# Performance work log

Hardware: AMD Instinct MI355X
Metric: run time of the kernel (lower is better)

## Reference

```python
import jax, jax.numpy as jnp
import numpy as np

N = 50000
E = 800000
IN_C = 16
H = 64
EA = 3
L = 3
EPS = 1e-5

def layer_norm(h, g, b):
    mu = jnp.mean(h, axis=-1, keepdims=True)
    var = jnp.var(h, axis=-1, keepdims=True)
    return (h - mu) * jax.lax.rsqrt(var + EPS) * g + b

def setup_inputs() -> dict:
    key = jax.random.key(0)
    ks = jax.random.split(key, 24)
    s = lambda *sh: 0.05
    d = {}
    d["x"] = jax.random.normal(ks[0], (N, IN_C), jnp.float32)
    d["edge_index"] = jax.random.randint(ks[1], (2, E), 0, N, jnp.int32)
    d["edge_attr"] = jax.random.normal(ks[2], (E, EA), jnp.float32)
    # encoder
    d["enc_w"] = jax.random.normal(ks[3], (IN_C, H), jnp.float32) * 0.1
    d["enc_b"] = jnp.zeros((H,), jnp.float32)
    d["enc_ln_g"] = jnp.ones((H,), jnp.float32)
    d["enc_ln_b"] = jnp.zeros((H,), jnp.float32)
    # message-passing MLPs (stacked over layers)
    d["mlp_w1"] = jax.random.normal(ks[4], (L, H + EA, H // 2), jnp.float32) * 0.1
    d["mlp_b1"] = jnp.zeros((L, H // 2), jnp.float32)
    d["mlp_w2"] = jax.random.normal(ks[5], (L, H // 2, H), jnp.float32) * 0.1
    d["mlp_b2"] = jnp.zeros((L, H), jnp.float32)
    d["ln_g"] = jnp.ones((L, H), jnp.float32)
    d["ln_b"] = jnp.zeros((L, H), jnp.float32)
    # heads
    d["depth_w1"] = jax.random.normal(ks[6], (H, H // 2), jnp.float32) * 0.1
    d["depth_b1"] = jnp.zeros((H // 2,), jnp.float32)
    d["depth_w2"] = jax.random.normal(ks[7], (H // 2, 1), jnp.float32) * 0.1
    d["depth_b2"] = jnp.zeros((1,), jnp.float32)
    d["vel_w1"] = jax.random.normal(ks[8], (H, H // 2), jnp.float32) * 0.1
    d["vel_b1"] = jnp.zeros((H // 2,), jnp.float32)
    d["vel_w2"] = jax.random.normal(ks[9], (H // 2, 2), jnp.float32) * 0.1
    d["vel_b2"] = jnp.zeros((2,), jnp.float32)
    return d

def reference(x, edge_index, edge_attr, enc_w, enc_b, enc_ln_g, enc_ln_b,
              mlp_w1, mlp_b1, mlp_w2, mlp_b2, ln_g, ln_b,
              depth_w1, depth_b1, depth_w2, depth_b2,
              vel_w1, vel_b1, vel_w2, vel_b2):
    src, dst = edge_index[0], edge_index[1]  # PyG: x_j = x[src], aggregate at dst
    # encoder (dropout inactive in eval mode)
    h = layer_norm(x @ enc_w + enc_b, enc_ln_g, enc_ln_b)
    h = jax.nn.relu(h)
    # in-degree counts for mean aggregation (isolated nodes -> 0, like PyG)
    cnt = jax.ops.segment_sum(jnp.ones((E,), jnp.float32), dst, num_segments=N)
    inv_cnt = jnp.where(cnt > 0, 1.0 / jnp.maximum(cnt, 1.0), 0.0)[:, None]
    for i in range(L):
        m_in = jnp.concatenate([h[src], edge_attr], axis=1)          # [E, H+EA]
        m = jax.nn.relu(m_in @ mlp_w1[i] + mlp_b1[i]) @ mlp_w2[i] + mlp_b2[i]  # [E, H]
        agg = jax.ops.segment_sum(m, dst, num_segments=N) * inv_cnt  # mean aggregate
        h = layer_norm(h + agg, ln_g[i], ln_b[i])
    depth = jax.nn.relu(h @ depth_w1 + depth_b1) @ depth_w2 + depth_b2    # [N,1]
    velocity = jax.nn.relu(h @ vel_w1 + vel_b1) @ vel_w2 + vel_b2         # [N,2]
    return (depth, velocity)
```

## Files before the change

kernel.cpp:

```cpp
#include <hip/hip_runtime.h>
#include <hip/hip_bf16.h>
#include <hip/hip_fp16.h>

typedef __hip_bfloat16 bf16;
typedef unsigned int u32;
typedef float f4v __attribute__((ext_vector_type(4)));

#define NN 50000
#define NE 800000
#define INC 16
#define HD 64
#define EPSV 1e-5f
#define NB1 196

__device__ __forceinline__ float b2f(bf16 v) { return __bfloat162float(v); }
__device__ __forceinline__ bool is_bf(const void* det) {
  return *(const u32*)det == 0x3F803F80u;
}

__device__ __forceinline__ float4 ldnt4(const float4* p) {
  f4v t = __builtin_nontemporal_load(reinterpret_cast<const f4v*>(p));
  float4 r; r.x = t[0]; r.y = t[1]; r.z = t[2]; r.w = t[3];
  return r;
}

template<typename T> __device__ __forceinline__ float ldv(const T* p, int i);
template<> __device__ __forceinline__ float ldv<float>(const float* p, int i) { return p[i]; }
template<> __device__ __forceinline__ float ldv<bf16>(const bf16* p, int i) { return b2f(p[i]); }

#define W1F   0
#define B1F   6432
#define W2F   6528
#define B2F   12672
#define DW1F  12864
#define DB1F  14912
#define DW2F  14944
#define DB2F  14976
#define VW1F  14977
#define VB1F  17025
#define VW2F  17057
#define VB2F  17121
#define WFTOT 17123

#define H_OFF    0
#define P0_OFF   3200000
#define CSR_OFF  4800000
#define WF_OFF   8000000
#define CNTI_OFF (WF_OFF + WFTOT)
#define RS_OFF   (CNTI_OFF + NN)
#define BSUM_OFF (RS_OFF + NN)
#define BOFF_OFF (BSUM_OFF + 256)
#define LPOS_OFF (BOFF_OFF + 256)
#define INV_OFF  (LPOS_OFF + NE)
#define P1_OFF   (INV_OFF + NE)
#define WS_NEED_ROOMY ((size_t)(P1_OFF + NN * 16) * 4)

template<typename T>
__device__ __forceinline__ void prep_body(
    const T* w1, const T* b1, const T* w2, const T* b2,
    const T* dw1, const T* db1, const T* dw2, const T* db2,
    const T* vw1, const T* vb1, const T* vw2, const T* vb2,
    float* wf, int i) {
  float v;
  if      (i < B1F)  v = ldv(w1,  i - W1F);
  else if (i < W2F)  v = ldv(b1,  i - B1F);
  else if (i < B2F)  v = ldv(w2,  i - W2F);
  else if (i < DW1F) v = ldv(b2,  i - B2F);
  else if (i < DB1F) v = ldv(dw1, i - DW1F);
  else if (i < DW2F) v = ldv(db1, i - DB1F);
  else if (i < DB2F) v = ldv(dw2, i - DW2F);
  else if (i < VW1F) v = ldv(db2, i - DB2F);
  else if (i < VB1F) v = ldv(vw1, i - VW1F);
  else if (i < VW2F) v = ldv(vb1, i - VB1F);
  else if (i < VB2F) v = ldv(vw2, i - VW2F);
  else               v = ldv(vb2, i - VB2F);
  wf[i] = v;
}

__global__ __launch_bounds__(256) void prep_kernel(
    const void* w1, const void* b1, const void* w2, const void* b2,
    const void* dw1, const void* db1, const void* dw2, const void* db2,
    const void* vw1, const void* vb1, const void* vw2, const void* vb2,
    float* __restrict__ wf, const void* __restrict__ det) {
  int i = blockIdx.x * blockDim.x + threadIdx.x;
  if (i >= WFTOT) return;
  if (is_bf(det))
    prep_body((const bf16*)w1, (const bf16*)b1, (const bf16*)w2, (const bf16*)b2,
              (const bf16*)dw1, (const bf16*)db1, (const bf16*)dw2, (const bf16*)db2,
              (const bf16*)vw1, (const bf16*)vb1, (const bf16*)vw2, (const bf16*)vb2, wf, i);
  else
    prep_body((const float*)w1, (const float*)b1, (const float*)w2, (const float*)b2,
              (const float*)dw1, (const float*)db1, (const float*)dw2, (const float*)db2,
              (const float*)vw1, (const float*)vb1, (const float*)vw2, (const float*)vb2, wf, i);
}

__global__ __launch_bounds__(256) void encoder_kernel(
    const void* __restrict__ x, const void* __restrict__ enc_w,
    const void* __restrict__ enc_b, const void* __restrict__ g,
    const void* __restrict__ b, float* __restrict__ h,
    __half* __restrict__ pout, const float* __restrict__ nw1,
    const float* __restrict__ nb1, const void* __restrict__ det) {
  __shared__ float shv[4][64];
  int node = (blockIdx.x * blockDim.x + threadIdx.x) >> 6;
  int lane = threadIdx.x & 63;
  int w = threadIdx.x >> 6;
  if (node >= NN) return;
  int jl = lane & 31, half = lane >> 5;
  float xv[INC], wv[INC], ebv, gv, bv;
  if (is_bf(det)) {
    const bf16* xp = (const bf16*)x + node * INC;
    const bf16* wp = (const bf16*)enc_w;
    #pragma unroll
    for (int k = 0; k < INC; k++) { xv[k] = b2f(xp[k]); wv[k] = b2f(wp[k * HD + lane]); }
    ebv = b2f(((const bf16*)enc_b)[lane]);
    gv  = b2f(((const bf16*)g)[lane]);
    bv  = b2f(((const bf16*)b)[lane]);
  } else {
    const float* xp = (const float*)x + node * INC;
    const float* wp = (const float*)enc_w;
    #pragma unroll
    for (int k = 0; k < INC; k++) { xv[k] = xp[k]; wv[k] = wp[k * HD + lane]; }
    ebv = ((const float*)enc_b)[lane];
    gv  = ((const float*)g)[lane];
    bv  = ((const float*)b)[lane];
  }
  float acc = ebv;
  #pragma unroll
  for (int k = 0; k < INC; k++) acc += xv[k] * wv[k];
  float s1 = acc, s2 = acc * acc;
  #pragma unroll
  for (int o = 32; o; o >>= 1) { s1 += __shfl_xor(s1, o); s2 += __shfl_xor(s2, o); }
  float mu = s1 * (1.0f / 64.0f);
  float var = fmaxf(s2 * (1.0f / 64.0f) - mu * mu, 0.0f);
  float d = acc - mu;
  float hv = fmaxf(d * rsqrtf(var + EPSV) * gv + bv, 0.0f);
  h[node * HD + lane] = hv;
  shv[w][lane] = hv;
  float pacc = 0.0f;
  int kb = half << 5;
  #pragma unroll
  for (int k4 = 0; k4 < 32; k4 += 4) {
    float4 h4 = *reinterpret_cast<const float4*>(&shv[w][kb + k4]);
    int kk = kb + k4;
    pacc += h4.x * nw1[kk * 32 + jl] + h4.y * nw1[(kk + 1) * 32 + jl]
          + h4.z * nw1[(kk + 2) * 32 + jl] + h4.w * nw1[(kk + 3) * 32 + jl];
  }
  pacc += __shfl_xor(pacc, 32);
  if (half == 0) pout[node * 32 + jl] = __float2half(pacc + nb1[jl]);
}

__global__ __launch_bounds__(256) void count_kernel(const int* __restrict__ ei,
                                                    int* __restrict__ cnt,
                                                    int* __restrict__ lpos) {
  int e = blockIdx.x * blockDim.x + threadIdx.x;
  if (e < NE) lpos[e] = atomicAdd(&cnt[ei[NE + e]], 1);
}

__global__ __launch_bounds__(256) void scan1_kernel(const int* __restrict__ cnt,
                                                    int* __restrict__ ex,
                                                    int* __restrict__ bsum) {
  __shared__ int s[256];
  int t = threadIdx.x, idx = blockIdx.x * 256 + t;
  int v = (idx < NN) ? cnt[idx] : 0;
  s[t] = v;
  __syncthreads();
  #pragma unroll
  for (int off = 1; off < 256; off <<= 1) {
    int u = (t >= off) ? s[t - off] : 0;
    __syncthreads();
    s[t] += u;
    __syncthreads();
  }
  if (idx < NN) ex[idx] = s[t] - v;
  if (t == 255) bsum[blockIdx.x] = s[255];
}

__global__ __launch_bounds__(256) void scan2_kernel(int* __restrict__ bsum,
                                                    int* __restrict__ boff) {
  __shared__ int s[256];
  int t = threadIdx.x;
  int v = (t < NB1) ? bsum[t] : 0;
  s[t] = v;
  __syncthreads();
  #pragma unroll
  for (int off = 1; off < 256; off <<= 1) {
    int u = (t >= off) ? s[t - off] : 0;
    __syncthreads();
    s[t] += u;
    __syncthreads();
  }
  boff[t] = s[t] - v;
}

__global__ __launch_bounds__(256) void scan3_kernel(int* __restrict__ rs,
                                                    const int* __restrict__ boff) {
  int idx = blockIdx.x * 256 + threadIdx.x;
  if (idx >= NN) return;
  rs[idx] += boff[blockIdx.x];
}

__global__ __launch_bounds__(256) void inv_kernel(const int* __restrict__ ei,
                                                  const int* __restrict__ rs,
                                                  const int* __restrict__ lpos,
                                                  int* __restrict__ inv) {
  int e = blockIdx.x * blockDim.x + threadIdx.x;
  if (e >= NE) return;
  int dst = ei[NE + e];
  inv[rs[dst] + lpos[e]] = e;
}

__global__ __launch_bounds__(256) void fill_kernel(const int* __restrict__ inv,
                                                   const int* __restrict__ ei,
                                                   const void* __restrict__ attr,
                                                   float4* __restrict__ csr,
                                                   const void* __restrict__ det) {
  int p = blockIdx.x * blockDim.x + threadIdx.x;
  if (p >= NE) return;
  int e = inv[p];
  int src = ei[e];
  float a0, a1, a2;
  if (is_bf(det)) {
    const bf16* ap = (const bf16*)attr + 3 * e;
    a0 = b2f(ap[0]); a1 = b2f(ap[1]); a2 = b2f(ap[2]);
  } else {
    const float* ap = (const float*)attr + 3 * e;
    a0 = ap[0]; a1 = ap[1]; a2 = ap[2];
  }
  float4 v; v.x = a0; v.y = a1; v.z = a2; v.w = __int_as_float(src);
  csr[p] = v;
}

__global__ __launch_bounds__(256) void node_pre_kernel(
    const float* __restrict__ h, const float* __restrict__ w1,
    const float* __restrict__ b1, __half* __restrict__ p) {
  int t = blockIdx.x * blockDim.x + threadIdx.x;
  int node = t >> 5;
  int j = t & 31;
  if (node >= NN) return;
  const float* hr = h + node * HD;
  float acc = b1[j];
  #pragma unroll
  for (int k = 0; k < HD; k++) acc += hr[k] * w1[k * 32 + j];
  p[node * 32 + j] = __float2half(acc);
}

__global__ __launch_bounds__(128) void gather_kernel(
    float* __restrict__ h, const __half2* __restrict__ pin,
    __half* __restrict__ pnext, const float4* __restrict__ csr,
    const int* __restrict__ rs, const int* __restrict__ cnt,
    const float* __restrict__ w1a, const float* __restrict__ w2,
    const float* __restrict__ b2v, const void* __restrict__ gbase,
    const void* __restrict__ bbase, int layer,
    const float* __restrict__ nw1, const float* __restrict__ nb1,
    int do_pnext, const float* __restrict__ wf, void* __restrict__ out,
    const void* __restrict__ det) {
  __shared__ float sacc[2][2][32];
  __shared__ float shv[2][2][64];
  int wid = (blockIdx.x * blockDim.x + threadIdx.x) >> 6;
  int lane = threadIdx.x & 63;
  int w = threadIdx.x >> 6;
  int n0 = 2 * wid, n1 = 2 * wid + 1;
  if (n0 >= NN) return;
  int jl = lane & 31, half = lane >> 5;
  int q4 = lane >> 4, pp = lane & 15;
  float2 wa0 = *reinterpret_cast<const float2*>(&w1a[2 * pp]);
  float2 wa1 = *reinterpret_cast<const float2*>(&w1a[32 + 2 * pp]);
  float2 wa2 = *reinterpret_cast<const float2*>(&w1a[64 + 2 * pp]);
  int s0 = rs[n0], c0 = cnt[n0];
  int s1 = rs[n1], c1 = cnt[n1];
  float hres0 = h[n0 * HD + lane];
  float hres1 = h[n1 * HD + lane];
  float b2l = b2v[lane];

  bool isbf = is_bf(det);
  int gidx = layer * HD + lane;
  float gv, bv;
  if (isbf) {
    gv = b2f(((const bf16*)gbase)[gidx]);
    bv = b2f(((const bf16*)bbase)[gidx]);
  } else {
    gv = ((const float*)gbase)[gidx];
    bv = ((const float*)bbase)[gidx];
  }

  int cm10 = (c0 > 0) ? c0 - 1 : 0;
  int cm11 = (c1 > 0) ? c1 - 1 : 0;
  int t0 = (c0 > 0) ? s0 : 0;
  int t1 = (c1 > 0) ? s1 : 0;

  float2 acc0 = make_float2(0.f, 0.f), acc1 = make_float2(0.f, 0.f);
  int cmax = max(c0, c1);
  if (cmax > 0) {
    float4 e0[4], e1[4];
    #pragma unroll
    for (int t = 0; t < 4; t++) {
      e0[t] = ldnt4(&csr[t0 + min(4 * t + q4, cm10)]);
      e1[t] = ldnt4(&csr[t1 + min(4 * t + q4, cm11)]);
    }
    for (int b0 = 0; b0 < cmax; b0 += 16) {
      float2 g0[4], g1[4];
      #pragma unroll
      for (int t = 0; t < 4; t++)
        g0[t] = __half22float2(pin[__float_as_int(e0[t].w) * 16 + pp]);
      #pragma unroll
      for (int t = 0; t < 4; t++)
        g1[t] = __half22float2(pin[__float_as_int(e1[t].w) * 16 + pp]);
      float2 pa0[4], pa1[4];
      #pragma unroll
      for (int t = 0; t < 4; t++) {
        pa0[t].x = e0[t].x * wa0.x + e0[t].y * wa1.x + e0[t].z * wa2.x;
        pa0[t].y = e0[t].x * wa0.y + e0[t].y * wa1.y + e0[t].z * wa2.y;
        pa1[t].x = e1[t].x * wa0.x + e1[t].y * wa1.x + e1[t].z * wa2.x;
        pa1[t].y = e1[t].x * wa0.y + e1[t].y * wa1.y + e1[t].z * wa2.y;
      }
      int nb = b0 + 16;
      if (nb < cmax) {
        #pragma unroll
        for (int t = 0; t < 4; t++) {
          e0[t] = ldnt4(&csr[t0 + min(nb + 4 * t + q4, cm10)]);
          e1[t] = ldnt4(&csr[t1 + min(nb + 4 * t + q4, cm11)]);
        }
      }
      #pragma unroll
      for (int t = 0; t < 4; t++) {
        int eo = b0 + 4 * t + q4;
        float rx0 = fmaxf(g0[t].x + pa0[t].x, 0.0f);
        float ry0 = fmaxf(g0[t].y + pa0[t].y, 0.0f);
        acc0.x += (eo < c0) ? rx0 : 0.0f;
        acc0.y += (eo < c0) ? ry0 : 0.0f;
        float rx1 = fmaxf(g1[t].x + pa1[t].x, 0.0f);
        float ry1 = fmaxf(g1[t].y + pa1[t].y, 0.0f);
        acc1.x += (eo < c1) ? rx1 : 0.0f;
        acc1.y += (eo < c1) ? ry1 : 0.0f;
      }
    }
  }
  acc0.x += __shfl_xor(acc0.x, 16); acc0.y += __shfl_xor(acc0.y, 16);
  acc1.x += __shfl_xor(acc1.x, 16); acc1.y += __shfl_xor(acc1.y, 16);
  acc0.x += __shfl_xor(acc0.x, 32); acc0.y += __shfl_xor(acc0.y, 32);
  acc1.x += __shfl_xor(acc1.x, 32); acc1.y += __shfl_xor(acc1.y, 32);
  if (lane < 16) {
    *reinterpret_cast<float2*>(&sacc[w][0][2 * pp]) = acc0;
    *reinterpret_cast<float2*>(&sacc[w][1][2 * pp]) = acc1;
  }

  float m0 = 0.0f, m1 = 0.0f;
  #pragma unroll
  for (int j4 = 0; j4 < 32; j4 += 4) {
    float4 a0 = *reinterpret_cast<const float4*>(&sacc[w][0][j4]);
    float4 a1 = *reinterpret_cast<const float4*>(&sacc[w][1][j4]);
    float w20 = w2[(j4 + 0) * HD + lane], w21 = w2[(j4 + 1) * HD + lane];
    float w22 = w2[(j4 + 2) * HD + lane], w23 = w2[(j4 + 3) * HD + lane];
    m0 += a0.x * w20 + a0.y * w21 + a0.z * w22 + a0.w * w23;
    m1 += a1.x * w20 + a1.y * w21 + a1.z * w22 + a1.w * w23;
  }
  float aggv0 = (c0 > 0) ? (m0 / (float)c0 + b2l) : 0.0f;
  float aggv1 = (c1 > 0) ? (m1 / (float)c1 + b2l) : 0.0f;

  float v0 = hres0 + aggv0, v1 = hres1 + aggv1;
  float s10 = v0, s20 = v0 * v0, s11 = v1, s21 = v1 * v1;
  #pragma unroll
  for (int o = 32; o; o >>= 1) {
    s10 += __shfl_xor(s10, o); s20 += __shfl_xor(s20, o);
    s11 += __shfl_xor(s11, o); s21 += __shfl_xor(s21, o);
  }
  float mu0 = s10 * (1.0f / 64.0f), mu1 = s11 * (1.0f / 64.0f);
  float var0 = fmaxf(s20 * (1.0f / 64.0f) - mu0 * mu0, 0.0f);
  float var1 = fmaxf(s21 * (1.0f / 64.0f) - mu1 * mu1, 0.0f);
  float hv0 = (v0 - mu0) * rsqrtf(var0 + EPSV) * gv + bv;
  float hv1 = (v1 - mu1) * rsqrtf(var1 + EPSV) * gv + bv;

  shv[w][0][lane] = hv0;
  shv[w][1][lane] = hv1;

  if (do_pnext) {
    float p0a = 0.0f, p1a = 0.0f;
    int kb = half << 5;
    #pragma unroll
    for (int k4 = 0; k4 < 32; k4 += 4) {
      float4 h0 = *reinterpret_cast<const float4*>(&shv[w][0][kb + k4]);
      float4 h1 = *reinterpret_cast<const float4*>(&shv[w][1][kb + k4]);
      int kk = kb + k4;
      float n0v = nw1[kk * 32 + jl], n1v = nw1[(kk + 1) * 32 + jl];
      float n2v = nw1[(kk + 2) * 32 + jl], n3v = nw1[(kk + 3) * 32 + jl];
      p0a += h0.x * n0v + h0.y * n1v + h0.z * n2v + h0.w * n3v;
      p1a += h1.x * n0v + h1.y * n1v + h1.z * n2v + h1.w * n3v;
    }
    p0a += __shfl_xor(p0a, 32);
    p1a += __shfl_xor(p1a, 32);
    if (half == 0) {
      pnext[n0 * 32 + jl] = __float2half(p0a + nb1[jl]);
      pnext[n1 * 32 + jl] = __float2half(p1a + nb1[jl]);
    }
  }

  if (layer == 2) {
    const float* w1h = wf + (half ? VW1F : DW1F);
    float a20 = half ? wf[VB1F + jl] : wf[DB1F + jl];
    float a21 = a20;
    #pragma unroll
    for (int k4 = 0; k4 < 64; k4 += 4) {
      float4 h0 = *reinterpret_cast<const float4*>(&shv[w][0][k4]);
      float4 h1 = *reinterpret_cast<const float4*>(&shv[w][1][k4]);
      float wv0 = w1h[(k4 + 0) * 32 + jl], wv1 = w1h[(k4 + 1) * 32 + jl];
      float wv2 = w1h[(k4 + 2) * 32 + jl], wv3 = w1h[(k4 + 3) * 32 + jl];
      a20 += h0.x * wv0 + h0.y * wv1 + h0.z * wv2 + h0.w * wv3;
      a21 += h1.x * wv0 + h1.y * wv1 + h1.z * wv2 + h1.w * wv3;
    }
    a20 = fmaxf(a20, 0.0f);
    a21 = fmaxf(a21, 0.0f);
    float r00, r10, r01, r11;
    if (half == 0) {
      r00 = a20 * wf[DW2F + jl]; r10 = 0.0f;
      r01 = a21 * wf[DW2F + jl]; r11 = 0.0f;
    } else {
      r00 = a20 * wf[VW2F + 2 * jl]; r10 = a20 * wf[VW2F + 2 * jl + 1];
      r01 = a21 * wf[VW2F + 2 * jl]; r11 = a21 * wf[VW2F + 2 * jl + 1];
    }
    #pragma unroll
    for (int o = 16; o; o >>= 1) {
      r00 += __shfl_xor(r00, o); r10 += __shfl_xor(r10, o);
      r01 += __shfl_xor(r01, o); r11 += __shfl_xor(r11, o);
    }
    if (lane == 0) {
      float d0 = r00 + wf[DB2F];
      float d1 = r01 + wf[DB2F];
      if (isbf) {
        ((bf16*)out)[n0] = __float2bfloat16(d0);
        ((bf16*)out)[n1] = __float2bfloat16(d1);
      } else {
        ((float*)out)[n0] = d0;
        ((float*)out)[n1] = d1;
      }
    }
    if (lane == 32) {
      float v00 = r00 + wf[VB2F], v01 = r10 + wf[VB2F + 1];
      float v10 = r01 + wf[VB2F], v11 = r11 + wf[VB2F + 1];
      if (isbf) {
        ((bf16*)out)[NN + 2 * n0]     = __float2bfloat16(v00);
        ((bf16*)out)[NN + 2 * n0 + 1] = __float2bfloat16(v01);
        ((bf16*)out)[NN + 2 * n1]     = __float2bfloat16(v10);
        ((bf16*)out)[NN + 2 * n1 + 1] = __float2bfloat16(v11);
      } else {
        ((float*)out)[NN + 2 * n0]     = v00;
        ((float*)out)[NN + 2 * n0 + 1] = v01;
        ((float*)out)[NN + 2 * n1]     = v10;
        ((float*)out)[NN + 2 * n1 + 1] = v11;
      }
    }
  } else {
    h[n0 * HD + lane] = hv0;
    h[n1 * HD + lane] = hv1;
  }
}

extern "C" void kernel_launch(void* const* d_in, const int* in_sizes, int n_in,
                              void* d_out, int out_size, void* d_ws, size_t ws_size,
                              hipStream_t stream) {
  const void* x     = d_in[0];
  const int*  ei    = (const int*)d_in[1];
  const void* attr  = d_in[2];
  const void* enc_w = d_in[3];
  const void* enc_b = d_in[4];
  const void* enc_g = d_in[5];
  const void* enc_bb= d_in[6];
  const void* mw1   = d_in[7];
  const void* mb1   = d_in[8];
  const void* mw2   = d_in[9];
  const void* mb2   = d_in[10];
  const void* lng   = d_in[11];
  const void* lnb   = d_in[12];
  const void* dw1   = d_in[13];
  const void* db1   = d_in[14];
  const void* dw2   = d_in[15];
  const void* db2   = d_in[16];
  const void* vw1   = d_in[17];
  const void* vb1   = d_in[18];
  const void* vw2   = d_in[19];
  const void* vb2   = d_in[20];

  float* ws    = (float*)d_ws;
  float* h     = ws + H_OFF;
  __half* p0   = (__half*)(ws + P0_OFF);
  float4* csr  = (float4*)(ws + CSR_OFF);
  float* wf    = ws + WF_OFF;
  int*   cnti  = (int*)(ws + CNTI_OFF);
  int*   rs    = (int*)(ws + RS_OFF);
  int*   bsum  = (int*)(ws + BSUM_OFF);
  int*   boff  = (int*)(ws + BOFF_OFF);
  int*   lpos  = (int*)(ws + LPOS_OFF);
  int*   inv   = (int*)(ws + INV_OFF);
  __half* p1   = (__half*)(ws + P1_OFF);
  bool roomy = ws_size >= WS_NEED_ROOMY;

  hipMemsetAsync(cnti, 0, (size_t)NN * sizeof(int), stream);
  prep_kernel<<<(WFTOT + 255) / 256, 256, 0, stream>>>(
      mw1, mb1, mw2, mb2, dw1, db1, dw2, db2, vw1, vb1, vw2, vb2, wf, enc_g);
  encoder_kernel<<<(NN + 3) / 4, 256, 0, stream>>>(
      x, enc_w, enc_b, enc_g, enc_bb, h, p0, wf + W1F, wf + B1F, enc_g);
  count_kernel<<<(NE + 255) / 256, 256, 0, stream>>>(ei, cnti, lpos);
  scan1_kernel<<<NB1, 256, 0, stream>>>(cnti, rs, bsum);
  scan2_kernel<<<1, 256, 0, stream>>>(bsum, boff);
  scan3_kernel<<<NB1, 256, 0, stream>>>(rs, boff);
  inv_kernel<<<(NE + 255) / 256, 256, 0, stream>>>(ei, rs, lpos, inv);
  fill_kernel<<<(NE + 255) / 256, 256, 0, stream>>>(inv, ei, attr, csr, enc_g);

  for (int l = 0; l < 3; l++) {
    __half* pin  = (roomy && (l & 1)) ? p1 : p0;
    __half* pnxt = (roomy && !(l & 1)) ? p1 : p0;
    if (!roomy && l > 0) {
      node_pre_kernel<<<(NN * 32 + 255) / 256, 256, 0, stream>>>(
          h, wf + W1F + l * 2144, wf + B1F + l * 32, p0);
      pin = p0; pnxt = p0;
    }
    int do_pnext = (roomy && l < 2) ? 1 : 0;
    int nl = (l < 2) ? l + 1 : l;
    gather_kernel<<<(NN + 3) / 4, 128, 0, stream>>>(
        h, (const __half2*)pin, pnxt, csr, rs, cnti,
        wf + W1F + l * 2144 + 64 * 32, wf + W2F + l * 2048, wf + B2F + l * 64,
        lng, lnb, l,
        wf + W1F + nl * 2144, wf + B1F + nl * 32, do_pnext,
        wf, d_out, enc_g);
  }
}
```

Before: 344.9 us.

## Process four nodes per wavefront in gather and fuse count into encoder

The gather kernel now handles four destination nodes per 64-lane wavefront instead of two, with 256-thread blocks, vectorized int4 loads of row starts and counts, and 16 outstanding CSR/gather loads per lane for more memory-level parallelism. The in-degree count kernel is merged into the encoder launch as extra blocks, removing one launch and letting the two independent jobs overlap. The trade-offs are higher register pressure (which may lower occupancy) and more divergence from unequal degrees, since each wave loops to the largest degree of its four nodes.

Result: slower. 478.3 us (+38.7%).

```diff
diff --git a/kernel.cpp b/kernel.cpp
--- a/kernel.cpp
+++ b/kernel.cpp
@@ -12,6 +12,8 @@
 #define HD 64
 #define EPSV 1e-5f
 #define NB1 196
+#define CNTB 3125
+#define ENCB 12500
 
 __device__ __forceinline__ float b2f(bf16 v) { return __bfloat162float(v); }
 __device__ __forceinline__ bool is_bf(const void* det) {
@@ -94,14 +96,21 @@
               (const float*)vw1, (const float*)vb1, (const float*)vw2, (const float*)vb2, wf, i);
 }
 
-__global__ __launch_bounds__(256) void encoder_kernel(
+__global__ __launch_bounds__(256) void enc_count_kernel(
     const void* __restrict__ x, const void* __restrict__ enc_w,
     const void* __restrict__ enc_b, const void* __restrict__ g,
     const void* __restrict__ b, float* __restrict__ h,
     __half* __restrict__ pout, const float* __restrict__ nw1,
-    const float* __restrict__ nb1, const void* __restrict__ det) {
+    const float* __restrict__ nb1, const int* __restrict__ ei,
+    int* __restrict__ cnt, int* __restrict__ lpos,
+    const void* __restrict__ det) {
+  if (blockIdx.x < CNTB) {
+    int e = blockIdx.x * 256 + threadIdx.x;
+    if (e < NE) lpos[e] = atomicAdd(&cnt[ei[NE + e]], 1);
+    return;
+  }
   __shared__ float shv[4][64];
-  int node = (blockIdx.x * blockDim.x + threadIdx.x) >> 6;
+  int node = ((blockIdx.x - CNTB) * blockDim.x + threadIdx.x) >> 6;
   int lane = threadIdx.x & 63;
   int w = threadIdx.x >> 6;
   if (node >= NN) return;
@@ -147,13 +156,6 @@
   }
   pacc += __shfl_xor(pacc, 32);
   if (half == 0) pout[node * 32 + jl] = __float2half(pacc + nb1[jl]);
-}
-
-__global__ __launch_bounds__(256) void count_kernel(const int* __restrict__ ei,
-                                                    int* __restrict__ cnt,
-                                                    int* __restrict__ lpos) {
-  int e = blockIdx.x * blockDim.x + threadIdx.x;
-  if (e < NE) lpos[e] = atomicAdd(&cnt[ei[NE + e]], 1);
 }
 
 __global__ __launch_bounds__(256) void scan1_kernel(const int* __restrict__ cnt,
@@ -244,7 +246,7 @@
   p[node * 32 + j] = __float2half(acc);
 }
 
-__global__ __launch_bounds__(128) void gather_kernel(
+__global__ __launch_bounds__(256) void gather_kernel(
     float* __restrict__ h, const __half2* __restrict__ pin,
     __half* __restrict__ pnext, const float4* __restrict__ csr,
     const int* __restrict__ rs, const int* __restrict__ cnt,
@@ -254,22 +256,25 @@
     const float* __restrict__ nw1, const float* __restrict__ nb1,
     int do_pnext, const float* __restrict__ wf, void* __restrict__ out,
     const void* __restrict__ det) {
-  __shared__ float sacc[2][2][32];
-  __shared__ float shv[2][2][64];
+  __shared__ float sacc[4][4][32];
+  __shared__ float shv[4][4][64];
   int wid = (blockIdx.x * blockDim.x + threadIdx.x) >> 6;
   int lane = threadIdx.x & 63;
   int w = threadIdx.x >> 6;
-  int n0 = 2 * wid, n1 = 2 * wid + 1;
+  int n0 = 4 * wid;
   if (n0 >= NN) return;
   int jl = lane & 31, half = lane >> 5;
   int q4 = lane >> 4, pp = lane & 15;
   float2 wa0 = *reinterpret_cast<const float2*>(&w1a[2 * pp]);
   float2 wa1 = *reinterpret_cast<const float2*>(&w1a[32 + 2 * pp]);
   float2 wa2 = *reinterpret_cast<const float2*>(&w1a[64 + 2 * pp]);
-  int s0 = rs[n0], c0 = cnt[n0];
-  int s1 = rs[n1], c1 = cnt[n1];
-  float hres0 = h[n0 * HD + lane];
-  float hres1 = h[n1 * HD + lane];
+  int4 s4 = *reinterpret_cast<const int4*>(&rs[n0]);
+  int4 c4 = *reinterpret_cast<const int4*>(&cnt[n0]);
+  int sA[4] = {s4.x, s4.y, s4.z, s4.w};
+  int cA[4] = {c4.x, c4.y, c4.z, c4.w};
+  float hres[4];
+  #pragma unroll
+  for (int n = 0; n < 4; n++) hres[n] = h[(n0 + n) * HD + lane];
   float b2l = b2v[lane];
 
   bool isbf = is_bf(det);
@@ -283,174 +288,192 @@
     bv = ((const float*)bbase)[gidx];
   }
 
-  int cm10 = (c0 > 0) ? c0 - 1 : 0;
-  int cm11 = (c1 > 0) ? c1 - 1 : 0;
-  int t0 = (c0 > 0) ? s0 : 0;
-  int t1 = (c1 > 0) ? s1 : 0;
-
-  float2 acc0 = make_float2(0.f, 0.f), acc1 = make_float2(0.f, 0.f);
-  int cmax = max(c0, c1);
+  int tA[4], cmA[4];
+  #pragma unroll
+  for (int n = 0; n < 4; n++) {
+    cmA[n] = (cA[n] > 0) ? cA[n] - 1 : 0;
+    tA[n]  = (cA[n] > 0) ? sA[n] : 0;
+  }
+
+  float2 acc[4];
+  #pragma unroll
+  for (int n = 0; n < 4; n++) acc[n] = make_float2(0.f, 0.f);
+  int cmax = max(max(cA[0], cA[1]), max(cA[2], cA[3]));
   if (cmax > 0) {
-    float4 e0[4], e1[4];
-    #pragma unroll
-    for (int t = 0; t < 4; t++) {
-      e0[t] = ldnt4(&csr[t0 + min(4 * t + q4, cm10)]);
-      e1[t] = ldnt4(&csr[t1 + min(4 * t + q4, cm11)]);
+    float4 e[4][4];
+    #pragma unroll
+    for (int n = 0; n < 4; n++) {
+      #pragma unroll
+      for (int t = 0; t < 4; t++)
+        e[n][t] = ldnt4(&csr[tA[n] + min(4 * t + q4, cmA[n])]);
     }
     for (int b0 = 0; b0 < cmax; b0 += 16) {
-      float2 g0[4], g1[4];
-      #pragma unroll
-      for (int t = 0; t < 4; t++)
-        g0[t] = __half22float2(pin[__float_as_int(e0[t].w) * 16 + pp]);
-      #pragma unroll
-      for (int t = 0; t < 4; t++)
-        g1[t] = __half22float2(pin[__float_as_int(e1[t].w) * 16 + pp]);
-      float2 pa0[4], pa1[4];
-      #pragma unroll
-      for (int t = 0; t < 4; t++) {
-        pa0[t].x = e0[t].x * wa0.x + e0[t].y * wa1.x + e0[t].z * wa2.x;
-        pa0[t].y = e0[t].x * wa0.y + e0[t].y * wa1.y + e0[t].z * wa2.y;
-        pa1[t].x = e1[t].x * wa0.x + e1[t].y * wa1.x + e1[t].z * wa2.x;
-        pa1[t].y = e1[t].x * wa0.y + e1[t].y * wa1.y + e1[t].z * wa2.y;
+      float2 g[4][4];
+      #pragma unroll
+      for (int n = 0; n < 4; n++) {
+        #pragma unroll
+        for (int t = 0; t < 4; t++)
+          g[n][t] = __half22float2(pin[__float_as_int(e[n][t].w) * 16 + pp]);
+      }
+      float2 pa[4][4];
+      #pragma unroll
+      for (int n = 0; n < 4; n++) {
+        #pragma unroll
+        for (int t = 0; t < 4; t++) {
+          pa[n][t].x = e[n][t].x * wa0.x + e[n][t].y * wa1.x + e[n][t].z * wa2.x;
+          pa[n][t].y = e[n][t].x * wa0.y + e[n][t].y * wa1.y + e[n][t].z * wa2.y;
+        }
       }
       int nb = b0 + 16;
       if (nb < cmax) {
         #pragma unroll
+        for (int n = 0; n < 4; n++) {
+          #pragma unroll
+          for (int t = 0; t < 4; t++)
+            e[n][t] = ldnt4(&csr[tA[n] + min(nb + 4 * t + q4, cmA[n])]);
+        }
+      }
+      #pragma unroll
+      for (int n = 0; n < 4; n++) {
+        #pragma unroll
         for (int t = 0; t < 4; t++) {
-          e0[t] = ldnt4(&csr[t0 + min(nb + 4 * t + q4, cm10)]);
-          e1[t] = ldnt4(&csr[t1 + min(nb + 4 * t + q4, cm11)]);
+          int eo = b0 + 4 * t + q4;
+          float rx = fmaxf(g[n][t].x + pa[n][t].x, 0.0f);
+          float ry = fmaxf(g[n][t].y + pa[n][t].y, 0.0f);
+          acc[n].x += (eo < cA[n]) ? rx : 0.0f;
+          acc[n].y += (eo < cA[n]) ? ry : 0.0f;
         }
       }
-      #pragma unroll
-      for (int t = 0; t < 4; t++) {
-        int eo = b0 + 4 * t + q4;
-        float rx0 = fmaxf(g0[t].x + pa0[t].x, 0.0f);
-        float ry0 = fmaxf(g0[t].y + pa0[t].y, 0.0f);
-        acc0.x += (eo < c0) ? rx0 : 0.0f;
-        acc0.y += (eo < c0) ? ry0 : 0.0f;
-        float rx1 = fmaxf(g1[t].x + pa1[t].x, 0.0f);
-        float ry1 = fmaxf(g1[t].y + pa1[t].y, 0.0f);
-        acc1.x += (eo < c1) ? rx1 : 0.0f;
-        acc1.y += (eo < c1) ? ry1 : 0.0f;
-      }
-    }
-  }
-  acc0.x += __shfl_xor(acc0.x, 16); acc0.y += __shfl_xor(acc0.y, 16);
-  acc1.x += __shfl_xor(acc1.x, 16); acc1.y += __shfl_xor(acc1.y, 16);
-  acc0.x += __shfl_xor(acc0.x, 32); acc0.y += __shfl_xor(acc0.y, 32);
-  acc1.x += __shfl_xor(acc1.x, 32); acc1.y += __shfl_xor(acc1.y, 32);
+    }
+  }
+  #pragma unroll
+  for (int n = 0; n < 4; n++) {
+    acc[n].x += __shfl_xor(acc[n].x, 16); acc[n].y += __shfl_xor(acc[n].y, 16);
+  }
+  #pragma unroll
+  for (int n = 0; n < 4; n++) {
+    acc[n].x += __shfl_xor(acc[n].x, 32); acc[n].y += __shfl_xor(acc[n].y, 32);
+  }
   if (lane < 16) {
-    *reinterpret_cast<float2*>(&sacc[w][0][2 * pp]) = acc0;
-    *reinterpret_cast<float2*>(&sacc[w][1][2 * pp]) = acc1;
-  }
-
-  float m0 = 0.0f, m1 = 0.0f;
+    #pragma unroll
+    for (int n = 0; n < 4; n++)
+      *reinterpret_cast<float2*>(&sacc[w][n][2 * pp]) = acc[n];
+  }
+
+  float m[4] = {0.f, 0.f, 0.f, 0.f};
   #pragma unroll
   for (int j4 = 0; j4 < 32; j4 += 4) {
-    float4 a0 = *reinterpret_cast<const float4*>(&sacc[w][0][j4]);
-    float4 a1 = *reinterpret_cast<const float4*>(&sacc[w][1][j4]);
     float w20 = w2[(j4 + 0) * HD + lane], w21 = w2[(j4 + 1) * HD + lane];
     float w22 = w2[(j4 + 2) * HD + lane], w23 = w2[(j4 + 3) * HD + lane];
-    m0 += a0.x * w20 + a0.y * w21 + a0.z * w22 + a0.w * w23;
-    m1 += a1.x * w20 + a1.y * w21 + a1.z * w22 + a1.w * w23;
-  }
-  float aggv0 = (c0 > 0) ? (m0 / (float)c0 + b2l) : 0.0f;
-  float aggv1 = (c1 > 0) ? (m1 / (float)c1 + b2l) : 0.0f;
-
-  float v0 = hres0 + aggv0, v1 = hres1 + aggv1;
-  float s10 = v0, s20 = v0 * v0, s11 = v1, s21 = v1 * v1;
+    #pragma unroll
+    for (int n = 0; n < 4; n++) {
+      float4 a = *reinterpret_cast<const float4*>(&sacc[w][n][j4]);
+      m[n] += a.x * w20 + a.y * w21 + a.z * w22 + a.w * w23;
+    }
+  }
+
+  float v[4], s1v[4], s2v[4];
+  #pragma unroll
+  for (int n = 0; n < 4; n++) {
+    float aggv = (cA[n] > 0) ? (m[n] / (float)cA[n] + b2l) : 0.0f;
+    v[n] = hres[n] + aggv;
+    s1v[n] = v[n]; s2v[n] = v[n] * v[n];
+  }
   #pragma unroll
   for (int o = 32; o; o >>= 1) {
-    s10 += __shfl_xor(s10, o); s20 += __shfl_xor(s20, o);
-    s11 += __shfl_xor(s11, o); s21 += __shfl_xor(s21, o);
-  }
-  float mu0 = s10 * (1.0f / 64.0f), mu1 = s11 * (1.0f / 64.0f);
-  float var0 = fmaxf(s20 * (1.0f / 64.0f) - mu0 * mu0, 0.0f);
-  float var1 = fmaxf(s21 * (1.0f / 64.0f) - mu1 * mu1, 0.0f);
-  float hv0 = (v0 - mu0) * rsqrtf(var0 + EPSV) * gv + bv;
-  float hv1 = (v1 - mu1) * rsqrtf(var1 + EPSV) * gv + bv;
-
-  shv[w][0][lane] = hv0;
-  shv[w][1][lane] = hv1;
+    #pragma unroll
+    for (int n = 0; n < 4; n++) {
+      s1v[n] += __shfl_xor(s1v[n], o);
+      s2v[n] += __shfl_xor(s2v[n], o);
+    }
+  }
+  float hv[4];
+  #pragma unroll
+  for (int n = 0; n < 4; n++) {
+    float mu = s1v[n] * (1.0f / 64.0f);
+    float var = fmaxf(s2v[n] * (1.0f / 64.0f) - mu * mu, 0.0f);
+    hv[n] = (v[n] - mu) * rsqrtf(var + EPSV) * gv + bv;
+    shv[w][n][lane] = hv[n];
+  }
 
   if (do_pnext) {
-    float p0a = 0.0f, p1a = 0.0f;
+    float pacc[4] = {0.f, 0.f, 0.f, 0.f};
     int kb = half << 5;
     #pragma unroll
     for (int k4 = 0; k4 < 32; k4 += 4) {
-      float4 h0 = *reinterpret_cast<const float4*>(&shv[w][0][kb + k4]);
-      float4 h1 = *reinterpret_cast<const float4*>(&shv[w][1][kb + k4]);
       int kk = kb + k4;
-      float n0v = nw1[kk * 32 + jl], n1v = nw1[(kk + 1) * 32 + jl];
+      float n0v = nw1[kk * 32 + jl],       n1v = nw1[(kk + 1) * 32 + jl];
       float n2v = nw1[(kk + 2) * 32 + jl], n3v = nw1[(kk + 3) * 32 + jl];
-      p0a += h0.x * n0v + h0.y * n1v + h0.z * n2v + h0.w * n3v;
-      p1a += h1.x * n0v + h1.y * n1v + h1.z * n2v + h1.w * n3v;
-    }
-    p0a += __shfl_xor(p0a, 32);
-    p1a += __shfl_xor(p1a, 32);
+      #pragma unroll
+      for (int n = 0; n < 4; n++) {
+        float4 hh = *reinterpret_cast<const float4*>(&shv[w][n][kb + k4]);
+        pacc[n] += hh.x * n0v + hh.y * n1v + hh.z * n2v + hh.w * n3v;
+      }
+    }
+    #pragma unroll
+    for (int n = 0; n < 4; n++) pacc[n] += __shfl_xor(pacc[n], 32);
     if (half == 0) {
-      pnext[n0 * 32 + jl] = __float2half(p0a + nb1[jl]);
-      pnext[n1 * 32 + jl] = __float2half(p1a + nb1[jl]);
+      #pragma unroll
+      for (int n = 0; n < 4; n++)
+        pnext[(n0 + n) * 32 + jl] = __float2half(pacc[n] + nb1[jl]);
     }
   }
 
   if (layer == 2) {
     const float* w1h = wf + (half ? VW1F : DW1F);
-    float a20 = half ? wf[VB1F + jl] : wf[DB1F + jl];
-    float a21 = a20;
+    float bias = half ? wf[VB1F + jl] : wf[DB1F + jl];
+    float a2[4] = {bias, bias, bias, bias};
     #pragma unroll
     for (int k4 = 0; k4 < 64; k4 += 4) {
-      float4 h0 = *reinterpret_cast<const float4*>(&shv[w][0][k4]);
-      float4 h1 = *reinterpret_cast<const float4*>(&shv[w][1][k4]);
       float wv0 = w1h[(k4 + 0) * 32 + jl], wv1 = w1h[(k4 + 1) * 32 + jl];
       float wv2 = w1h[(k4 + 2) * 32 + jl], wv3 = w1h[(k4 + 3) * 32 + jl];
-      a20 += h0.x * wv0 + h0.y * wv1 + h0.z * wv2 + h0.w * wv3;
-      a21 += h1.x * wv0 + h1.y * wv1 + h1.z * wv2 + h1.w * wv3;
-    }
-    a20 = fmaxf(a20, 0.0f);
-    a21 = fmaxf(a21, 0.0f);
-    float r00, r10, r01, r11;
-    if (half == 0) {
-      r00 = a20 * wf[DW2F + jl]; r10 = 0.0f;
-      r01 = a21 * wf[DW2F + jl]; r11 = 0.0f;
-    } else {
-      r00 = a20 * wf[VW2F + 2 * jl]; r10 = a20 * wf[VW2F + 2 * jl + 1];
-      r01 = a21 * wf[VW2F + 2 * jl]; r11 = a21 * wf[VW2F + 2 * jl + 1];
+      #pragma unroll
+      for (int n = 0; n < 4; n++) {
+        float4 hh = *reinterpret_cast<const float4*>(&shv[w][n][k4]);
+        a2[n] += hh.x * wv0 + hh.y * wv1 + hh.z * wv2 + hh.w * wv3;
+      }
+    }
+    float wv2l = half ? wf[VW2F + 2 * jl] : wf[DW2F + jl];
+    float wv2h = half ? wf[VW2F + 2 * jl + 1] : 0.0f;
+    float r0[4], r1[4];
+    #pragma unroll
+    for (int n = 0; n < 4; n++) {
+      a2[n] = fmaxf(a2[n], 0.0f);
+      r0[n] = a2[n] * wv2l;
+      r1[n] = a2[n] * wv2h;
     }
     #pragma unroll
     for (int o = 16; o; o >>= 1) {
-      r00 += __shfl_xor(r00, o); r10 += __shfl_xor(r10, o);
-      r01 += __shfl_xor(r01, o); r11 += __shfl_xor(r11, o);
+      #pragma unroll
+      for (int n = 0; n < 4; n++) {
+        r0[n] += __shfl_xor(r0[n], o);
+        r1[n] += __shfl_xor(r1[n], o);
+      }
     }
     if (lane == 0) {
-      float d0 = r00 + wf[DB2F];
-      float d1 = r01 + wf[DB2F];
-      if (isbf) {
-        ((bf16*)out)[n0] = __float2bfloat16(d0);
-        ((bf16*)out)[n1] = __float2bfloat16(d1);
-      } else {
-        ((float*)out)[n0] = d0;
-        ((float*)out)[n1] = d1;
+      #pragma unroll
+      for (int n = 0; n < 4; n++) {
+        float d0 = r0[n] + wf[DB2F];
+        if (isbf) ((bf16*)out)[n0 + n] = __float2bfloat16(d0);
+        else      ((float*)out)[n0 + n] = d0;
       }
     }
     if (lane == 32) {
-      float v00 = r00 + wf[VB2F], v01 = r10 + wf[VB2F + 1];
-      float v10 = r01 + wf[VB2F], v11 = r11 + wf[VB2F + 1];
-      if (isbf) {
-        ((bf16*)out)[NN + 2 * n0]     = __float2bfloat16(v00);
-        ((bf16*)out)[NN + 2 * n0 + 1] = __float2bfloat16(v01);
-        ((bf16*)out)[NN + 2 * n1]     = __float2bfloat16(v10);
-        ((bf16*)out)[NN + 2 * n1 + 1] = __float2bfloat16(v11);
-      } else {
-        ((float*)out)[NN + 2 * n0]     = v00;
-        ((float*)out)[NN + 2 * n0 + 1] = v01;
-        ((float*)out)[NN + 2 * n1]     = v10;
-        ((float*)out)[NN + 2 * n1 + 1] = v11;
+      #pragma unroll
+      for (int n = 0; n < 4; n++) {
+        float v0 = r0[n] + wf[VB2F], v1 = r1[n] + wf[VB2F + 1];
+        if (isbf) {
+          ((bf16*)out)[NN + 2 * (n0 + n)]     = __float2bfloat16(v0);
+          ((bf16*)out)[NN + 2 * (n0 + n) + 1] = __float2bfloat16(v1);
+        } else {
+          ((float*)out)[NN + 2 * (n0 + n)]     = v0;
+          ((float*)out)[NN + 2 * (n0 + n) + 1] = v1;
+        }
       }
     }
   } else {
-    h[n0 * HD + lane] = hv0;
-    h[n1 * HD + lane] = hv1;
+    #pragma unroll
+    for (int n = 0; n < 4; n++) h[(n0 + n) * HD + lane] = hv[n];
   }
 }
 
@@ -496,9 +519,9 @@
   hipMemsetAsync(cnti, 0, (size_t)NN * sizeof(int), stream);
   prep_kernel<<<(WFTOT + 255) / 256, 256, 0, stream>>>(
       mw1, mb1, mw2, mb2, dw1, db1, dw2, db2, vw1, vb1, vw2, vb2, wf, enc_g);
-  encoder_kernel<<<(NN + 3) / 4, 256, 0, stream>>>(
-      x, enc_w, enc_b, enc_g, enc_bb, h, p0, wf + W1F, wf + B1F, enc_g);
-  count_kernel<<<(NE + 255) / 256, 256, 0, stream>>>(ei, cnti, lpos);
+  enc_count_kernel<<<CNTB + ENCB, 256, 0, stream>>>(
+      x, enc_w, enc_b, enc_g, enc_bb, h, p0, wf + W1F, wf + B1F,
+      ei, cnti, lpos, enc_g);
   scan1_kernel<<<NB1, 256, 0, stream>>>(cnti, rs, bsum);
   scan2_kernel<<<1, 256, 0, stream>>>(bsum, boff);
   scan3_kernel<<<NB1, 256, 0, stream>>>(rs, boff);
@@ -515,7 +538,7 @@
     }
     int do_pnext = (roomy && l < 2) ? 1 : 0;
     int nl = (l < 2) ? l + 1 : l;
-    gather_kernel<<<(NN + 3) / 4, 128, 0, stream>>>(
+    gather_kernel<<<(NN + 15) / 16, 256, 0, stream>>>(
         h, (const __half2*)pin, pnxt, csr, rs, cnti,
         wf + W1F + l * 2144 + 64 * 32, wf + W2F + l * 2048, wf + B2F + l * 64,
         lng, lnb, l,
```

## Pack CSR edge records to 8 bytes and fuse degree count into encoder

Applied to the files above, without the earlier changes.

Each CSR edge entry shrinks from a float4 (three fp32 attributes plus an int source) to a uint2 holding three fp16 attributes and a 16-bit source index. This halves the streamed edge bytes the gather kernel reads in each layer. The standalone count kernel is folded into the encoder launch as extra leading blocks, which removes one launch and lets the atomic counting overlap with encoder work. The cost is lower precision on the edge attributes and a hard limit of 65536 nodes for the source index.

New measurement: 340.8 us. Within noise of the previous version (-1.2%).

```diff
diff --git a/kernel.cpp b/kernel.cpp
--- a/kernel.cpp
+++ b/kernel.cpp
@@ -4,7 +4,7 @@
 
 typedef __hip_bfloat16 bf16;
 typedef unsigned int u32;
-typedef float f4v __attribute__((ext_vector_type(4)));
+typedef unsigned int u2v __attribute__((ext_vector_type(2)));
 
 #define NN 50000
 #define NE 800000
@@ -12,15 +12,17 @@
 #define HD 64
 #define EPSV 1e-5f
 #define NB1 196
+#define CNTB 3125
+#define ENCB 12500
 
 __device__ __forceinline__ float b2f(bf16 v) { return __bfloat162float(v); }
 __device__ __forceinline__ bool is_bf(const void* det) {
   return *(const u32*)det == 0x3F803F80u;
 }
 
-__device__ __forceinline__ float4 ldnt4(const float4* p) {
-  f4v t = __builtin_nontemporal_load(reinterpret_cast<const f4v*>(p));
-  float4 r; r.x = t[0]; r.y = t[1]; r.z = t[2]; r.w = t[3];
+__device__ __forceinline__ uint2 ldnt2(const uint2* p) {
+  u2v t = __builtin_nontemporal_load(reinterpret_cast<const u2v*>(p));
+  uint2 r; r.x = t[0]; r.y = t[1];
   return r;
 }
 
@@ -94,14 +96,21 @@
               (const float*)vw1, (const float*)vb1, (const float*)vw2, (const float*)vb2, wf, i);
 }
 
-__global__ __launch_bounds__(256) void encoder_kernel(
+__global__ __launch_bounds__(256) void enc_count_kernel(
     const void* __restrict__ x, const void* __restrict__ enc_w,
     const void* __restrict__ enc_b, const void* __restrict__ g,
     const void* __restrict__ b, float* __restrict__ h,
     __half* __restrict__ pout, const float* __restrict__ nw1,
-    const float* __restrict__ nb1, const void* __restrict__ det) {
+    const float* __restrict__ nb1, const int* __restrict__ ei,
+    int* __restrict__ cnt, int* __restrict__ lpos,
+    const void* __restrict__ det) {
+  if (blockIdx.x < CNTB) {
+    int e = blockIdx.x * 256 + threadIdx.x;
+    if (e < NE) lpos[e] = atomicAdd(&cnt[ei[NE + e]], 1);
+    return;
+  }
   __shared__ float shv[4][64];
-  int node = (blockIdx.x * blockDim.x + threadIdx.x) >> 6;
+  int node = ((blockIdx.x - CNTB) * blockDim.x + threadIdx.x) >> 6;
   int lane = threadIdx.x & 63;
   int w = threadIdx.x >> 6;
   if (node >= NN) return;
@@ -149,13 +158,6 @@
   if (half == 0) pout[node * 32 + jl] = __float2half(pacc + nb1[jl]);
 }
 
-__global__ __launch_bounds__(256) void count_kernel(const int* __restrict__ ei,
-                                                    int* __restrict__ cnt,
-                                                    int* __restrict__ lpos) {
-  int e = blockIdx.x * blockDim.x + threadIdx.x;
-  if (e < NE) lpos[e] = atomicAdd(&cnt[ei[NE + e]], 1);
-}
-
 __global__ __launch_bounds__(256) void scan1_kernel(const int* __restrict__ cnt,
                                                     int* __restrict__ ex,
                                                     int* __restrict__ bsum) {
@@ -212,12 +214,12 @@
 __global__ __launch_bounds__(256) void fill_kernel(const int* __restrict__ inv,
                                                    const int* __restrict__ ei,
                                                    const void* __restrict__ attr,
-                                                   float4* __restrict__ csr,
+                                                   uint2* __restrict__ csr,
                                                    const void* __restrict__ det) {
   int p = blockIdx.x * blockDim.x + threadIdx.x;
   if (p >= NE) return;
   int e = inv[p];
-  int src = ei[e];
+  u32 src = (u32)ei[e];
   float a0, a1, a2;
   if (is_bf(det)) {
     const bf16* ap = (const bf16*)attr + 3 * e;
@@ -226,7 +228,10 @@
     const float* ap = (const float*)attr + 3 * e;
     a0 = ap[0]; a1 = ap[1]; a2 = ap[2];
   }
-  float4 v; v.x = a0; v.y = a1; v.z = a2; v.w = __int_as_float(src);
+  u32 lo = ((u32)__half_as_ushort(__float2half(a1)) << 16)
+         | (u32)__half_as_ushort(__float2half(a0));
+  u32 hi = (src << 16) | (u32)__half_as_ushort(__float2half(a2));
+  uint2 v; v.x = lo; v.y = hi;
   csr[p] = v;
 }
 
@@ -246,7 +251,7 @@
 
 __global__ __launch_bounds__(128) void gather_kernel(
     float* __restrict__ h, const __half2* __restrict__ pin,
-    __half* __restrict__ pnext, const float4* __restrict__ csr,
+    __half* __restrict__ pnext, const uint2* __restrict__ csr,
     const int* __restrict__ rs, const int* __restrict__ cnt,
     const float* __restrict__ w1a, const float* __restrict__ w2,
     const float* __restrict__ b2v, const void* __restrict__ gbase,
@@ -291,34 +296,38 @@
   float2 acc0 = make_float2(0.f, 0.f), acc1 = make_float2(0.f, 0.f);
   int cmax = max(c0, c1);
   if (cmax > 0) {
-    float4 e0[4], e1[4];
+    uint2 e0[4], e1[4];
     #pragma unroll
     for (int t = 0; t < 4; t++) {
-      e0[t] = ldnt4(&csr[t0 + min(4 * t + q4, cm10)]);
-      e1[t] = ldnt4(&csr[t1 + min(4 * t + q4, cm11)]);
+      e0[t] = ldnt2(&csr[t0 + min(4 * t + q4, cm10)]);
+      e1[t] = ldnt2(&csr[t1 + min(4 * t + q4, cm11)]);
     }
     for (int b0 = 0; b0 < cmax; b0 += 16) {
       float2 g0[4], g1[4];
       #pragma unroll
       for (int t = 0; t < 4; t++)
-        g0[t] = __half22float2(pin[__float_as_int(e0[t].w) * 16 + pp]);
+        g0[t] = __half22float2(pin[(e0[t].y >> 16) * 16 + pp]);
       #pragma unroll
       for (int t = 0; t < 4; t++)
-        g1[t] = __half22float2(pin[__float_as_int(e1[t].w) * 16 + pp]);
+        g1[t] = __half22float2(pin[(e1[t].y >> 16) * 16 + pp]);
       float2 pa0[4], pa1[4];
       #pragma unroll
       for (int t = 0; t < 4; t++) {
-        pa0[t].x = e0[t].x * wa0.x + e0[t].y * wa1.x + e0[t].z * wa2.x;
-        pa0[t].y = e0[t].x * wa0.y + e0[t].y * wa1.y + e0[t].z * wa2.y;
-        pa1[t].x = e1[t].x * wa0.x + e1[t].y * wa1.x + e1[t].z * wa2.x;
-        pa1[t].y = e1[t].x * wa0.y + e1[t].y * wa1.y + e1[t].z * wa2.y;
+        float2 a01 = __half22float2(*reinterpret_cast<const __half2*>(&e0[t].x));
+        float a2 = __half2float(__ushort_as_half((unsigned short)(e0[t].y & 0xFFFFu)));
+        pa0[t].x = a01.x * wa0.x + a01.y * wa1.x + a2 * wa2.x;
+        pa0[t].y = a01.x * wa0.y + a01.y * wa1.y + a2 * wa2.y;
+        float2 b01 = __half22float2(*reinterpret_cast<const __half2*>(&e1[t].x));
+        float b2 = __half2float(__ushort_as_half((unsigned short)(e1[t].y & 0xFFFFu)));
+        pa1[t].x = b01.x * wa0.x + b01.y * wa1.x + b2 * wa2.x;
+        pa1[t].y = b01.x * wa0.y + b01.y * wa1.y + b2 * wa2.y;
       }
       int nb = b0 + 16;
       if (nb < cmax) {
         #pragma unroll
         for (int t = 0; t < 4; t++) {
-          e0[t] = ldnt4(&csr[t0 + min(nb + 4 * t + q4, cm10)]);
-          e1[t] = ldnt4(&csr[t1 + min(nb + 4 * t + q4, cm11)]);
+          e0[t] = ldnt2(&csr[t0 + min(nb + 4 * t + q4, cm10)]);
+          e1[t] = ldnt2(&csr[t1 + min(nb + 4 * t + q4, cm11)]);
         }
       }
       #pragma unroll
@@ -482,7 +491,7 @@
   float* ws    = (float*)d_ws;
   float* h     = ws + H_OFF;
   __half* p0   = (__half*)(ws + P0_OFF);
-  float4* csr  = (float4*)(ws + CSR_OFF);
+  uint2* csr   = (uint2*)(ws + CSR_OFF);
   float* wf    = ws + WF_OFF;
   int*   cnti  = (int*)(ws + CNTI_OFF);
   int*   rs    = (int*)(ws + RS_OFF);
@@ -496,9 +505,9 @@
   hipMemsetAsync(cnti, 0, (size_t)NN * sizeof(int), stream);
   prep_kernel<<<(WFTOT + 255) / 256, 256, 0, stream>>>(
       mw1, mb1, mw2, mb2, dw1, db1, dw2, db2, vw1, vb1, vw2, vb2, wf, enc_g);
-  encoder_kernel<<<(NN + 3) / 4, 256, 0, stream>>>(
-      x, enc_w, enc_b, enc_g, enc_bb, h, p0, wf + W1F, wf + B1F, enc_g);
-  count_kernel<<<(NE + 255) / 256, 256, 0, stream>>>(ei, cnti, lpos);
+  enc_count_kernel<<<CNTB + ENCB, 256, 0, stream>>>(
+      x, enc_w, enc_b, enc_g, enc_bb, h, p0, wf + W1F, wf + B1F,
+      ei, cnti, lpos, enc_g);
   scan1_kernel<<<NB1, 256, 0, stream>>>(cnti, rs, bsum);
   scan2_kernel<<<1, 256, 0, stream>>>(bsum, boff);
   scan3_kernel<<<NB1, 256, 0, stream>>>(rs, boff);
```
